# Optimization experiments

Measured on AMD Instinct MI355X. Metric: run time of the kernel, lower is better.

## Reference

```python
import jax, jax.numpy as jnp
import numpy as np
from jax import lax

LAG_SEQ = np.array([1, 2, 3, 7, 14, 28])   # original lags (steps back, newest-first indexing)
MAX_LAG = 28
N_LAGS = LAG_SEQ.size
CTX = 168          # context_length
H_PRED = 24        # prediction horizon H
HID = 512          # LSTM hidden dim
C_IN = 3           # raw channels: target + 2 covariates
IN_DIM = C_IN + 1 + N_LAGS   # + log(scale) feature + lag features = 10
OUT_DIM = 1
B = 512
L = MAX_LAG + CTX + H_PRED - 1   # 219


def setup_inputs() -> dict:
    key = jax.random.key(0)
    ks = jax.random.split(key, 9)
    s = 1.0 / np.sqrt(HID)
    u = lambda k, shape: jax.random.uniform(k, shape, jnp.float32, -s, s)
    return {
        "X": jax.random.normal(ks[0], (B, L, C_IN), jnp.float32),
        "pad_mask": jnp.ones((B, L), jnp.bool_),
        "H": H_PRED,
        "context_length": CTX,
        "W_ih0": u(ks[1], (4 * HID, IN_DIM)),
        "W_hh0": u(ks[2], (4 * HID, HID)),
        "b0": u(ks[3], (4 * HID,)),
        "W_ih1": u(ks[4], (4 * HID, HID)),
        "W_hh1": u(ks[5], (4 * HID, HID)),
        "b1": u(ks[6], (4 * HID,)),
        "W_head": u(ks[7], (HID, OUT_DIM)),
        "b_head": u(ks[8], (OUT_DIM,)),
    }


def _cell(x, h, c, W_ih, W_hh, b):
    # standard torch LSTM cell, gate order i,f,g,o
    g = x @ W_ih.T + h @ W_hh.T + b
    i, f, gg, o = jnp.split(g, 4, axis=-1)
    c = jax.nn.sigmoid(f) * c + jax.nn.sigmoid(i) * jnp.tanh(gg)
    h = jax.nn.sigmoid(o) * jnp.tanh(c)
    return h, c


def reference(X, pad_mask, H, context_length, W_ih0, W_hh0, b0, W_ih1, W_hh1, b1, W_head, b_head):
    Bx = X.shape[0]
    ctx = context_length
    h_steps = H - 1
    # zero out future targets (feature 0); covariates stay known in the future
    X = X.at[:, -h_steps:, 0].set(0.0)
    past = X[:, : X.shape[1] - h_steps, 0][:, ::-1]      # [B, MAX_LAG+ctx], newest-first
    Xs = X[:, MAX_LAG:]                                  # [B, T, C_IN], T = ctx + H - 1
    T = Xs.shape[1]
    m = pad_mask[:, MAX_LAG:][:, :ctx].astype(Xs.dtype)
    # masked mean-abs scaling over the context window of the target channel
    scale = (jnp.abs(Xs[:, :ctx, 0]) * m).sum(1) / jnp.maximum(m.sum(1), 1.0)
    scale = jnp.maximum(scale, 1e-3)[:, None, None]      # [B,1,1]
    past = past / scale[:, :, 0]
    Xcat = jnp.concatenate(
        [Xs[:, :, :1] / scale, Xs[:, :, 1:], jnp.broadcast_to(jnp.log(scale), (Bx, T, 1))],
        axis=2,
    )                                                    # [B, T, C_IN+1]
    # encoder lag features (vectorized create_lags + flip):
    # row i gathers newest-first past at indices LAG_SEQ + (ctx-1-i)
    idx = (ctx - 1 - np.arange(ctx))[:, None] + LAG_SEQ[None, :]   # [ctx, N_LAGS]
    lags = past[:, idx]                                  # [B, ctx, N_LAGS]
    enc_in = jnp.concatenate([Xcat[:, :ctx], lags], axis=2)        # [B, ctx, IN_DIM]

    z = jnp.zeros((Bx, HID), X.dtype)

    def enc_step(carry, x_t):
        h1, c1, h2, c2 = carry
        h1, c1 = _cell(x_t, h1, c1, W_ih0, W_hh0, b0)
        h2, c2 = _cell(h1, h2, c2, W_ih1, W_hh1, b1)
        return (h1, c1, h2, c2), h2

    carry, hs = lax.scan(enc_step, (z, z, z, z), enc_in.transpose(1, 0, 2))
    y_enc = hs.transpose(1, 0, 2) @ W_head + b_head      # [B, ctx, 1]

    covs = Xcat[:, ctx:, 1:].transpose(1, 0, 2)          # [H-1, B, C_IN]
    buf0 = past[:, : MAX_LAG + 1]                        # newest-first target buffer

    def dec_step(carry, cov_t):
        h1, c1, h2, c2, buf, pred = carry
        buf = jnp.concatenate([pred[:, None], buf[:, :-1]], axis=1)
        lag = buf[:, LAG_SEQ]                            # [B, N_LAGS]
        x_t = jnp.concatenate([pred[:, None], cov_t, lag], axis=1)  # [B, IN_DIM]
        h1, c1 = _cell(x_t, h1, c1, W_ih0, W_hh0, b0)
        h2, c2 = _cell(h1, h2, c2, W_ih1, W_hh1, b1)
        y = h2 @ W_head + b_head                         # [B, 1]
        return (h1, c1, h2, c2, buf, y[:, 0]), y

    _, ys = lax.scan(dec_step, (*carry, buf0, y_enc[:, -1, 0]), covs)
    y_dec = ys.transpose(1, 0, 2)                        # [B, H-1, 1]
    return jnp.concatenate([y_enc, y_dec], axis=1) * scale
```

## Files before the change

### kernel.cpp

```cpp
#include <hip/hip_runtime.h>

typedef unsigned short u16;
typedef unsigned int   u32;
typedef __bf16 bf16x8 __attribute__((ext_vector_type(8)));
typedef float  f32x4  __attribute__((ext_vector_type(4)));
static_assert(sizeof(bf16x8) == 16, "bf16x8 size");

#define NL   219
#define NOUT 191

__device__ const int LAGS[6] = {1, 2, 3, 7, 14, 28};

#define OFF_P0H 0UL
#define OFF_P0L (OFF_P0H + 2097152UL)
#define OFF_P1H (OFF_P0L + 2097152UL)
#define OFF_P1L (OFF_P1H + 4194304UL)
#define OFF_H1H (OFF_P1L + 4194304UL)
#define OFF_H1L (OFF_H1H + 1048576UL)
#define OFF_H2H (OFF_H1L + 1048576UL)
#define OFF_H2L (OFF_H2H + 1048576UL)
#define OFF_H2F (OFF_H2L + 1048576UL)
#define OFF_C1  (OFF_H2F + 2097152UL)
#define OFF_C2  (OFF_C1  + 1048576UL)
#define OFF_XF  (OFF_C2  + 1048576UL)
#define OFF_SC  (OFF_XF  + 3440640UL)
#define OFF_LS  (OFF_SC  + 2048UL)
#define OFF_VAL (OFF_LS  + 2048UL)
#define WS_NEED (OFF_VAL + 106496UL)
#define HPAR 262144UL

#define WSPTRS \
  u16*  p0h = (u16*)(ws + OFF_P0H); \
  u16*  p0l = (u16*)(ws + OFF_P0L); \
  u16*  p1h = (u16*)(ws + OFF_P1H); \
  u16*  p1l = (u16*)(ws + OFF_P1L); \
  u16*  h1h = (u16*)(ws + OFF_H1H); \
  u16*  h1l = (u16*)(ws + OFF_H1L); \
  u16*  h2h = (u16*)(ws + OFF_H2H); \
  u16*  h2l = (u16*)(ws + OFF_H2L); \
  float* h2f = (float*)(ws + OFF_H2F); \
  float* c1  = (float*)(ws + OFF_C1); \
  float* c2  = (float*)(ws + OFF_C2); \
  float* xf  = (float*)(ws + OFF_XF); \
  float* scp = (float*)(ws + OFF_SC); \
  float* lsp = (float*)(ws + OFF_LS); \
  float* valp = (float*)(ws + OFF_VAL); \
  (void)p0h;(void)p0l;(void)p1h;(void)p1l;(void)h1h;(void)h1l;(void)h2h;(void)h2l; \
  (void)h2f;(void)c1;(void)c2;(void)xf;(void)scp;(void)lsp;(void)valp;

__device__ __forceinline__ float sigm(float x){ return 1.f / (1.f + __expf(-x)); }
__device__ __forceinline__ float tanhx(float x){
  float ax = fabsf(x);
  float t  = __expf(-2.f * ax);
  float r  = (1.f - t) / (1.f + t);
  return copysignf(r, x);
}
__device__ __forceinline__ u16 f2bf(float x){
  u32 u = __float_as_uint(x);
  return (u16)((u + 0x7FFFu + ((u >> 16) & 1u)) >> 16);
}
__device__ __forceinline__ float bf2f(u16 h){ return __uint_as_float(((u32)h) << 16); }

template<int MF, int KB>
__device__ __forceinline__ void cell_mfma(
    const u16* __restrict__ AhiA, const u16* __restrict__ AloA,
    const u16* __restrict__ AhiB, const u16* __restrict__ AloB,
    const u16* __restrict__ phi,  const u16* __restrict__ plo,
    int R0, int jt, const float* __restrict__ bias,
    f32x4 (&acc)[MF][4])
{
  const int lane = threadIdx.x & 63;
  const int lrow = lane & 15;
  #pragma unroll
  for (int nf = 0; nf < 4; nf++){
    float bv = bias[nf * 512 + jt * 16 + lrow];
    f32x4 v = {bv, bv, bv, bv};
    #pragma unroll
    for (int mf = 0; mf < MF; mf++) acc[mf][nf] = v;
  }
  const size_t alo = (size_t)(lane >> 4) * 8;
  const size_t pb0 = (size_t)(jt * 4) * KB * 512 + (size_t)lane * 8;
  #pragma unroll 2
  for (int kb = 0; kb < KB; kb++){
    const u16* Ah; const u16* Al; int kl;
    if (KB == 16 || kb < 16){ Ah = AhiA; Al = AloA; kl = kb; }
    else                     { Ah = AhiB; Al = AloB; kl = kb - 16; }
    bf16x8 ah[MF], al[MF];
    #pragma unroll
    for (int mf = 0; mf < MF; mf++){
      size_t ao = (size_t)(R0 + mf * 16 + lrow) * 512 + (size_t)kl * 32 + alo;
      ah[mf] = *(const bf16x8*)(Ah + ao);
      al[mf] = *(const bf16x8*)(Al + ao);
    }
    bf16x8 bh[4], bl[4];
    #pragma unroll
    for (int nf = 0; nf < 4; nf++){
      size_t bo = pb0 + ((size_t)nf * KB + kb) * 512;
      bh[nf] = *(const bf16x8*)(phi + bo);
      bl[nf] = *(const bf16x8*)(plo + bo);
    }
    #pragma unroll
    for (int mf = 0; mf < MF; mf++){
      #pragma unroll
      for (int nf = 0; nf < 4; nf++){
        acc[mf][nf] = __builtin_amdgcn_mfma_f32_16x16x32_bf16(ah[mf], bh[nf], acc[mf][nf], 0, 0, 0);
        acc[mf][nf] = __builtin_amdgcn_mfma_f32_16x16x32_bf16(ah[mf], bl[nf], acc[mf][nf], 0, 0, 0);
        acc[mf][nf] = __builtin_amdgcn_mfma_f32_16x16x32_bf16(al[mf], bh[nf], acc[mf][nf], 0, 0, 0);
      }
    }
  }
}

template<int MF, bool XP>
__device__ __forceinline__ void cell_epi(
    f32x4 (&acc)[MF][4], int wrowbase, int m0, int jt,
    const float* xSl, const float* WihSl,
    float* __restrict__ cst,
    u16* __restrict__ hhd, u16* __restrict__ hld, float* __restrict__ hfd)
{
  const int lane = threadIdx.x & 63;
  const int lrow = lane & 15, lkb = lane >> 4;
  const int j = jt * 16 + lrow;
  #pragma unroll
  for (int mf = 0; mf < MF; mf++){
    #pragma unroll
    for (int r = 0; r < 4; r++){
      int lr = wrowbase + mf * 16 + lkb * 4 + r;
      int b  = m0 + lr;
      float gi = acc[mf][0][r], gf = acc[mf][1][r], gg = acc[mf][2][r], go = acc[mf][3][r];
      if (XP){
        #pragma unroll
        for (int k = 0; k < 10; k++){
          float xv = xSl[lr * 10 + k];
          gi += xv * WihSl[(0 * 16 + lrow) * 10 + k];
          gf += xv * WihSl[(1 * 16 + lrow) * 10 + k];
          gg += xv * WihSl[(2 * 16 + lrow) * 10 + k];
          go += xv * WihSl[(3 * 16 + lrow) * 10 + k];
        }
      }
      size_t ci = ((size_t)b << 9) + j;
      float co = cst[ci];
      float cn = sigm(gf) * co + sigm(gi) * tanhx(gg);
      float h  = sigm(go) * tanhx(cn);
      cst[ci] = cn;
      u16 hh = f2bf(h);
      hhd[ci] = hh;
      hld[ci] = f2bf(h - bf2f(hh));
      if (hfd) hfd[ci] = h;
    }
  }
}

__global__ __launch_bounds__(256) void prep1(
    const float* __restrict__ X, const float* __restrict__ Whh0,
    const float* __restrict__ Wih1, const float* __restrict__ Whh1,
    unsigned char* ws)
{
  WSPTRS
  __shared__ float redS[4];
  const int tid = threadIdx.x, w = blockIdx.x;
  const int gtid = w * 256 + tid, G = 65536;
  for (int i = gtid; i < 524288; i += G){ h1h[i] = 0; h1l[i] = 0; h2h[i] = 0; h2l[i] = 0; h2f[i] = 0.f; }
  for (int i = gtid; i < 262144; i += G){ c1[i] = 0.f; c2[i] = 0.f; }
  {
    int rowb = w * 2 + (tid >> 7);
    int t0 = tid & 127;
    float a = fabsf(X[((size_t)rowb * NL + 28 + t0) * 3]);
    if (t0 < 40) a += fabsf(X[((size_t)rowb * NL + 156 + t0) * 3]);
    #pragma unroll
    for (int off = 1; off < 64; off <<= 1) a += __shfl_xor(a, off, 64);
    if ((tid & 63) == 0) redS[tid >> 6] = a;
    __syncthreads();
    if (tid == 0 || tid == 128){
      float s = redS[tid >> 6] + redS[(tid >> 6) + 1];
      float sc = fmaxf(s / 168.f, 0.001f);
      scp[rowb] = sc; lsp[rowb] = logf(sc);
    }
  }
  for (int idx = gtid; idx < 1048576; idx += G){
    int e = idx & 7, ln = (idx >> 3) & 63, kb = (idx >> 9) & 15, nt = idx >> 13;
    int n = (nt & 3) * 512 + (nt >> 2) * 16 + (ln & 15);
    int k = kb * 32 + (ln >> 4) * 8 + e;
    float wv = Whh0[(size_t)n * 512 + k];
    u16 hh = f2bf(wv);
    p0h[idx] = hh; p0l[idx] = f2bf(wv - bf2f(hh));
  }
  for (int idx = gtid; idx < 2097152; idx += G){
    int e = idx & 7, ln = (idx >> 3) & 63, kb = (idx >> 9) & 31, nt = idx >> 14;
    int n = (nt & 3) * 512 + (nt >> 2) * 16 + (ln & 15);
    int k = kb * 32 + (ln >> 4) * 8 + e;
    float wv = (k < 512) ? Wih1[(size_t)n * 512 + k] : Whh1[(size_t)n * 512 + (k - 512)];
    u16 hh = f2bf(wv);
    p1h[idx] = hh; p1l[idx] = f2bf(wv - bf2f(hh));
  }
}

__global__ __launch_bounds__(256) void prep2(const float* __restrict__ X, unsigned char* ws)
{
  WSPTRS
  const int gtid = blockIdx.x * 256 + threadIdx.x, G = 65536;
  for (int idx = gtid; idx < 860160; idx += G){
    int k = idx % 10; int r = idx / 10; int b = r & 511; int t = r >> 9;
    size_t xb = (size_t)b * NL;
    float v;
    if (k == 0)      v = X[(xb + 28 + t) * 3] / scp[b];
    else if (k < 3)  v = X[(xb + 28 + t) * 3 + k];
    else if (k == 3) v = lsp[b];
    else { int lag = LAGS[k - 4]; v = X[(xb + 28 + t - lag) * 3] / scp[b]; }
    xf[idx] = v;
  }
  for (int idx = gtid; idx < 512 * 28; idx += G){
    int b = idx / 28, v = idx % 28;
    valp[b * 52 + v] = X[((size_t)b * NL + 168 + v) * 3] / scp[b];
  }
}

__global__ __launch_bounds__(256) void enc_step(
    const float* __restrict__ Wih0, const float* __restrict__ b0,
    const float* __restrict__ b1,   const float* __restrict__ Whead,
    const float* __restrict__ bhead, float* __restrict__ out,
    unsigned char* ws, int p)
{
  WSPTRS
  __shared__ float xS[1280];
  __shared__ float WihS[640];
  __shared__ float WhS[512];
  const int tid = threadIdx.x, w = blockIdx.x, wave = tid >> 6, jt = w & 31;
  const int P = p & 1;
  if (w < 128){
    const int m0 = ((w >> 5) & 3) * 128;
    if ((w & 31) == 0 && p >= 2){
      for (int i = tid; i < 512; i += 256) WhS[i] = Whead[i];
      __syncthreads();
      int t = p - 2;
      int row = tid >> 1, q = tid & 1;
      int b = m0 + row;
      const float4* h4 = (const float4*)(h2f + (size_t)P * HPAR + ((size_t)b << 9) + q * 256);
      const float4* w4 = (const float4*)(WhS + q * 256);
      float s = 0.f;
      #pragma unroll 8
      for (int i = 0; i < 64; i++){ float4 a = h4[i], bw = w4[i]; s += a.x*bw.x + a.y*bw.y + a.z*bw.z + a.w*bw.w; }
      s += __shfl_xor(s, 1, 64);
      if (q == 0) out[(size_t)b * NOUT + t] = (s + bhead[0]) * scp[b];
    }
    if (p <= 167){
      for (int i = tid; i < 640; i += 256){
        int col = i / 10, k = i % 10;
        int n = (col >> 4) * 512 + jt * 16 + (col & 15);
        WihS[i] = Wih0[n * 10 + k];
      }
      for (int i = tid; i < 1280; i += 256) xS[i] = xf[(size_t)(p * 512 + m0) * 10 + i];
      __syncthreads();
      f32x4 acc[2][4];
      cell_mfma<2,16>(h1h + (size_t)(1 - P) * HPAR, h1l + (size_t)(1 - P) * HPAR, nullptr, nullptr,
                      p0h, p0l, m0 + wave * 32, jt, b0, acc);
      cell_epi<2,true>(acc, wave * 32, m0, jt, xS, WihS, c1,
                       h1h + (size_t)P * HPAR, h1l + (size_t)P * HPAR, nullptr);
    }
  } else {
    if (p >= 1){
      const int m0 = ((w >> 5) & 3) * 128;
      f32x4 acc[2][4];
      cell_mfma<2,32>(h1h + (size_t)(1 - P) * HPAR, h1l + (size_t)(1 - P) * HPAR,
                      h2h + (size_t)P * HPAR,       h2l + (size_t)P * HPAR,
                      p1h, p1l, m0 + wave * 32, jt, b1, acc);
      cell_epi<2,false>(acc, wave * 32, m0, jt, nullptr, nullptr, c2,
                        h2h + (size_t)(1 - P) * HPAR, h2l + (size_t)(1 - P) * HPAR,
                        h2f + (size_t)(1 - P) * HPAR);
    }
  }
}

__global__ __launch_bounds__(256) void dec_cell0(
    const float* __restrict__ X, const float* __restrict__ Wih0,
    const float* __restrict__ b0, const float* __restrict__ Whead,
    const float* __restrict__ bhead, float* __restrict__ out,
    unsigned char* ws, int d)
{
  WSPTRS
  __shared__ float xS[640];
  __shared__ float WihS[640];
  __shared__ float WhS[512];
  __shared__ float ylds[64];
  const int tid = threadIdx.x, w = blockIdx.x, wave = tid >> 6, jt = w & 31;
  const int m0 = (w >> 5) * 64;
  const int hp = (d + 1) & 1;
  for (int i = tid; i < 512; i += 256) WhS[i] = Whead[i];
  for (int i = tid; i < 640; i += 256){
    int col = i / 10, k = i % 10;
    int n = (col >> 4) * 512 + jt * 16 + (col & 15);
    WihS[i] = Wih0[n * 10 + k];
  }
  __syncthreads();
  {
    int row = tid >> 2, q = tid & 3;
    int b = m0 + row;
    const float4* h4 = (const float4*)(h2f + (size_t)hp * HPAR + ((size_t)b << 9) + q * 128);
    const float4* w4 = (const float4*)(WhS + q * 128);
    float s = 0.f;
    #pragma unroll 8
    for (int i = 0; i < 32; i++){ float4 a = h4[i], bw = w4[i]; s += a.x*bw.x + a.y*bw.y + a.z*bw.z + a.w*bw.w; }
    s += __shfl_xor(s, 1, 64); s += __shfl_xor(s, 2, 64);
    if (q == 0){
      float y = s + bhead[0];
      ylds[row] = y;
      if (jt == 0){
        out[(size_t)b * NOUT + 167 + d] = y * scp[b];
        valp[b * 52 + 28 + d] = y;
      }
    }
  }
  __syncthreads();
  if (tid < 64){
    int b = m0 + tid;
    size_t xb = (size_t)b * NL;
    float* xr = xS + tid * 10;
    xr[0] = ylds[tid];
    xr[1] = X[(xb + 196 + d) * 3 + 1];
    xr[2] = X[(xb + 196 + d) * 3 + 2];
    xr[3] = lsp[b];
    #pragma unroll
    for (int j2 = 0; j2 < 6; j2++) xr[4 + j2] = valp[b * 52 + 28 + d - LAGS[j2]];
  }
  __syncthreads();
  f32x4 acc[1][4];
  cell_mfma<1,16>(h1h + (size_t)hp * HPAR, h1l + (size_t)hp * HPAR, nullptr, nullptr,
                  p0h, p0l, m0 + wave * 16, jt, b0, acc);
  cell_epi<1,true>(acc, wave * 16, m0, jt, xS, WihS, c1,
                   h1h + (size_t)(d & 1) * HPAR, h1l + (size_t)(d & 1) * HPAR, nullptr);
}

__global__ __launch_bounds__(256) void dec_cell1(
    const float* __restrict__ b1, unsigned char* ws, int d)
{
  WSPTRS
  const int tid = threadIdx.x, w = blockIdx.x, wave = tid >> 6, jt = w & 31;
  const int m0 = (w >> 5) * 64;
  const int hp = (d + 1) & 1;
  f32x4 acc[1][4];
  cell_mfma<1,32>(h1h + (size_t)(d & 1) * HPAR, h1l + (size_t)(d & 1) * HPAR,
                  h2h + (size_t)hp * HPAR,      h2l + (size_t)hp * HPAR,
                  p1h, p1l, m0 + wave * 16, jt, b1, acc);
  cell_epi<1,false>(acc, wave * 16, m0, jt, nullptr, nullptr, c2,
                    h2h + (size_t)(d & 1) * HPAR, h2l + (size_t)(d & 1) * HPAR,
                    h2f + (size_t)(d & 1) * HPAR);
  (void)tid;
}

__global__ __launch_bounds__(256) void dec_headf(
    const float* __restrict__ Whead, const float* __restrict__ bhead,
    float* __restrict__ out, unsigned char* ws)
{
  WSPTRS
  __shared__ float WhS[512];
  const int tid = threadIdx.x;
  const int m0 = blockIdx.x * 64;
  for (int i = tid; i < 512; i += 256) WhS[i] = Whead[i];
  __syncthreads();
  int row = tid >> 2, q = tid & 3;
  int b = m0 + row;
  const float4* h4 = (const float4*)(h2f + ((size_t)b << 9) + q * 128);
  const float4* w4 = (const float4*)(WhS + q * 128);
  float s = 0.f;
  #pragma unroll 8
  for (int i = 0; i < 32; i++){ float4 a = h4[i], bw = w4[i]; s += a.x*bw.x + a.y*bw.y + a.z*bw.z + a.w*bw.w; }
  s += __shfl_xor(s, 1, 64); s += __shfl_xor(s, 2, 64);
  if (q == 0) out[(size_t)b * NOUT + 190] = (s + bhead[0]) * scp[b];
}

extern "C" void kernel_launch(void* const* d_in, const int* in_sizes, int n_in,
                              void* d_out, int out_size, void* d_ws, size_t ws_size,
                              hipStream_t stream) {
  (void)in_sizes; (void)n_in; (void)out_size;
  if (ws_size < WS_NEED) return;
  const float* X    = (const float*)d_in[0];
  const float* Wih0 = (const float*)d_in[4];
  const float* Whh0 = (const float*)d_in[5];
  const float* b0   = (const float*)d_in[6];
  const float* Wih1 = (const float*)d_in[7];
  const float* Whh1 = (const float*)d_in[8];
  const float* b1   = (const float*)d_in[9];
  const float* Wh   = (const float*)d_in[10];
  const float* bh   = (const float*)d_in[11];
  float* out = (float*)d_out;
  unsigned char* ws = (unsigned char*)d_ws;

  prep1<<<dim3(256), dim3(256), 0, stream>>>(X, Whh0, Wih1, Whh1, ws);
  prep2<<<dim3(256), dim3(256), 0, stream>>>(X, ws);
  for (int p = 0; p <= 168; p++)
    enc_step<<<dim3(256), dim3(256), 0, stream>>>(Wih0, b0, b1, Wh, bh, out, ws, p);
  for (int d = 0; d <= 22; d++){
    dec_cell0<<<dim3(256), dim3(256), 0, stream>>>(X, Wih0, b0, Wh, bh, out, ws, d);
    dec_cell1<<<dim3(256), dim3(256), 0, stream>>>(b1, ws, d);
  }
  dec_headf<<<dim3(8), dim3(256), 0, stream>>>(Wh, bh, out, ws);
}
```

Before: 7.255 ms.

## Fuse all LSTM steps into one persistent kernel with grid barriers and LDS-resident weights

Replaces about 215 per-timestep kernel launches with a single persistent 256-block kernel that advances the encoder and decoder steps using a software grid barrier built on atomics. Each block keeps its slice of the recurrent weights in LDS (all of layer 0, the hi half of layer 1) and holds the cell state in registers instead of global memory. The decoder now uses 2 M-fragments per wave, the same as the encoder. The aim is to remove launch overhead and repeated weight and cell-state traffic. In exchange it depends on all 256 blocks being co-resident, and the barrier has a spin timeout that could break correctness if it expires.

```diff
diff --git a/kernel.cpp b/kernel.cpp
--- a/kernel.cpp
+++ b/kernel.cpp
@@ -20,33 +20,13 @@
 #define OFF_H2H (OFF_H1L + 1048576UL)
 #define OFF_H2L (OFF_H2H + 1048576UL)
 #define OFF_H2F (OFF_H2L + 1048576UL)
-#define OFF_C1  (OFF_H2F + 2097152UL)
-#define OFF_C2  (OFF_C1  + 1048576UL)
-#define OFF_XF  (OFF_C2  + 1048576UL)
+#define OFF_XF  (OFF_H2F + 2097152UL)
 #define OFF_SC  (OFF_XF  + 3440640UL)
 #define OFF_LS  (OFF_SC  + 2048UL)
 #define OFF_VAL (OFF_LS  + 2048UL)
-#define WS_NEED (OFF_VAL + 106496UL)
+#define OFF_BAR (OFF_VAL + 106496UL)
+#define WS_NEED (OFF_BAR + 64UL)
 #define HPAR 262144UL
-
-#define WSPTRS \
-  u16*  p0h = (u16*)(ws + OFF_P0H); \
-  u16*  p0l = (u16*)(ws + OFF_P0L); \
-  u16*  p1h = (u16*)(ws + OFF_P1H); \
-  u16*  p1l = (u16*)(ws + OFF_P1L); \
-  u16*  h1h = (u16*)(ws + OFF_H1H); \
-  u16*  h1l = (u16*)(ws + OFF_H1L); \
-  u16*  h2h = (u16*)(ws + OFF_H2H); \
-  u16*  h2l = (u16*)(ws + OFF_H2L); \
-  float* h2f = (float*)(ws + OFF_H2F); \
-  float* c1  = (float*)(ws + OFF_C1); \
-  float* c2  = (float*)(ws + OFF_C2); \
-  float* xf  = (float*)(ws + OFF_XF); \
-  float* scp = (float*)(ws + OFF_SC); \
-  float* lsp = (float*)(ws + OFF_LS); \
-  float* valp = (float*)(ws + OFF_VAL); \
-  (void)p0h;(void)p0l;(void)p1h;(void)p1l;(void)h1h;(void)h1l;(void)h2h;(void)h2l; \
-  (void)h2f;(void)c1;(void)c2;(void)xf;(void)scp;(void)lsp;(void)valp;
 
 __device__ __forceinline__ float sigm(float x){ return 1.f / (1.f + __expf(-x)); }
 __device__ __forceinline__ float tanhx(float x){
@@ -61,33 +41,53 @@
 }
 __device__ __forceinline__ float bf2f(u16 h){ return __uint_as_float(((u32)h) << 16); }
 
-template<int MF, int KB>
-__device__ __forceinline__ void cell_mfma(
+__device__ __forceinline__ void gridbar(u32* bar, u32 target){
+  __syncthreads();
+  if (threadIdx.x == 0){
+    __threadfence();
+    u32 a = __hip_atomic_fetch_add(bar, 1u, __ATOMIC_ACQ_REL, __HIP_MEMORY_SCOPE_AGENT);
+    if (a == 255u){
+      __hip_atomic_store(bar, 0u, __ATOMIC_RELAXED, __HIP_MEMORY_SCOPE_AGENT);
+      __hip_atomic_fetch_add(bar + 1, 1u, __ATOMIC_RELEASE, __HIP_MEMORY_SCOPE_AGENT);
+    } else {
+      u32 sp = 0;
+      while (__hip_atomic_load(bar + 1, __ATOMIC_ACQUIRE, __HIP_MEMORY_SCOPE_AGENT) < target
+             && ++sp < (1u << 17))
+        __builtin_amdgcn_s_sleep(2);
+    }
+    __threadfence();
+  }
+  __syncthreads();
+}
+
+template<int KB>
+__device__ __forceinline__ void cell_mfma2(
     const u16* __restrict__ AhiA, const u16* __restrict__ AloA,
     const u16* __restrict__ AhiB, const u16* __restrict__ AloB,
-    const u16* __restrict__ phi,  const u16* __restrict__ plo,
-    int R0, int jt, const float* __restrict__ bias,
-    f32x4 (&acc)[MF][4])
+    const u16* bh_s, const u16* bl_s,
+    int R0, float4 bias4, f32x4 (&acc)[2][4])
 {
   const int lane = threadIdx.x & 63;
   const int lrow = lane & 15;
-  #pragma unroll
-  for (int nf = 0; nf < 4; nf++){
-    float bv = bias[nf * 512 + jt * 16 + lrow];
-    f32x4 v = {bv, bv, bv, bv};
-    #pragma unroll
-    for (int mf = 0; mf < MF; mf++) acc[mf][nf] = v;
+  {
+    const float* bp = (const float*)&bias4;
+    #pragma unroll
+    for (int nf = 0; nf < 4; nf++){
+      float bv = bp[nf];
+      f32x4 v = {bv, bv, bv, bv};
+      acc[0][nf] = v; acc[1][nf] = v;
+    }
   }
   const size_t alo = (size_t)(lane >> 4) * 8;
-  const size_t pb0 = (size_t)(jt * 4) * KB * 512 + (size_t)lane * 8;
-  #pragma unroll 2
+  const u32 bo0 = (u32)lane * 8;
+  #pragma unroll 4
   for (int kb = 0; kb < KB; kb++){
     const u16* Ah; const u16* Al; int kl;
     if (KB == 16 || kb < 16){ Ah = AhiA; Al = AloA; kl = kb; }
     else                     { Ah = AhiB; Al = AloB; kl = kb - 16; }
-    bf16x8 ah[MF], al[MF];
-    #pragma unroll
-    for (int mf = 0; mf < MF; mf++){
+    bf16x8 ah[2], al[2];
+    #pragma unroll
+    for (int mf = 0; mf < 2; mf++){
       size_t ao = (size_t)(R0 + mf * 16 + lrow) * 512 + (size_t)kl * 32 + alo;
       ah[mf] = *(const bf16x8*)(Ah + ao);
       al[mf] = *(const bf16x8*)(Al + ao);
@@ -95,12 +95,12 @@
     bf16x8 bh[4], bl[4];
     #pragma unroll
     for (int nf = 0; nf < 4; nf++){
-      size_t bo = pb0 + ((size_t)nf * KB + kb) * 512;
-      bh[nf] = *(const bf16x8*)(phi + bo);
-      bl[nf] = *(const bf16x8*)(plo + bo);
-    }
-    #pragma unroll
-    for (int mf = 0; mf < MF; mf++){
+      u32 off = ((u32)(nf * KB + kb) << 9) + bo0;
+      bh[nf] = *(const bf16x8*)(bh_s + off);
+      bl[nf] = *(const bf16x8*)(bl_s + off);
+    }
+    #pragma unroll
+    for (int mf = 0; mf < 2; mf++){
       #pragma unroll
       for (int nf = 0; nf < 4; nf++){
         acc[mf][nf] = __builtin_amdgcn_mfma_f32_16x16x32_bf16(ah[mf], bh[nf], acc[mf][nf], 0, 0, 0);
@@ -111,18 +111,17 @@
   }
 }
 
-template<int MF, bool XP>
-__device__ __forceinline__ void cell_epi(
-    f32x4 (&acc)[MF][4], int wrowbase, int m0, int jt,
+template<bool XP>
+__device__ __forceinline__ void cell_epi2(
+    f32x4 (&acc)[2][4], float (&creg)[8], int wrowbase, int m0, int jt,
     const float* xSl, const float* WihSl,
-    float* __restrict__ cst,
     u16* __restrict__ hhd, u16* __restrict__ hld, float* __restrict__ hfd)
 {
   const int lane = threadIdx.x & 63;
   const int lrow = lane & 15, lkb = lane >> 4;
   const int j = jt * 16 + lrow;
   #pragma unroll
-  for (int mf = 0; mf < MF; mf++){
+  for (int mf = 0; mf < 2; mf++){
     #pragma unroll
     for (int r = 0; r < 4; r++){
       int lr = wrowbase + mf * 16 + lkb * 4 + r;
@@ -138,11 +137,11 @@
           go += xv * WihSl[(3 * 16 + lrow) * 10 + k];
         }
       }
-      size_t ci = ((size_t)b << 9) + j;
-      float co = cst[ci];
+      float co = creg[mf * 4 + r];
       float cn = sigm(gf) * co + sigm(gi) * tanhx(gg);
       float h  = sigm(go) * tanhx(cn);
-      cst[ci] = cn;
+      creg[mf * 4 + r] = cn;
+      size_t ci = ((size_t)b << 9) + j;
       u16 hh = f2bf(h);
       hhd[ci] = hh;
       hld[ci] = f2bf(h - bf2f(hh));
@@ -151,17 +150,63 @@
   }
 }
 
-__global__ __launch_bounds__(256) void prep1(
-    const float* __restrict__ X, const float* __restrict__ Whh0,
+__global__ void initbar(unsigned char* ws){
+  if (threadIdx.x < 16) ((u32*)(ws + OFF_BAR))[threadIdx.x] = 0;
+}
+
+__global__ __launch_bounds__(256, 1) void deepar(
+    const float* __restrict__ X,    const float* __restrict__ Wih0,
+    const float* __restrict__ Whh0, const float* __restrict__ b0,
     const float* __restrict__ Wih1, const float* __restrict__ Whh1,
+    const float* __restrict__ b1,   const float* __restrict__ Whead,
+    const float* __restrict__ bhead, float* __restrict__ out,
     unsigned char* ws)
 {
-  WSPTRS
+  __shared__ u16   BW[65536];
+  __shared__ float xS[1280];
+  __shared__ float WihS[640];
+  __shared__ float WhS[512];
+  __shared__ float ylds[128];
   __shared__ float redS[4];
-  const int tid = threadIdx.x, w = blockIdx.x;
-  const int gtid = w * 256 + tid, G = 65536;
+
+  u16*  p0h = (u16*)(ws + OFF_P0H);
+  u16*  p0l = (u16*)(ws + OFF_P0L);
+  u16*  p1h = (u16*)(ws + OFF_P1H);
+  u16*  p1l = (u16*)(ws + OFF_P1L);
+  u16*  h1h = (u16*)(ws + OFF_H1H);
+  u16*  h1l = (u16*)(ws + OFF_H1L);
+  u16*  h2h = (u16*)(ws + OFF_H2H);
+  u16*  h2l = (u16*)(ws + OFF_H2L);
+  float* h2f = (float*)(ws + OFF_H2F);
+  float* xf  = (float*)(ws + OFF_XF);
+  float* scp = (float*)(ws + OFF_SC);
+  float* lsp = (float*)(ws + OFF_LS);
+  float* valp = (float*)(ws + OFF_VAL);
+  u32*  bar = (u32*)(ws + OFF_BAR);
+
+  const int tid  = threadIdx.x;
+  const int w    = blockIdx.x;
+  const int wave = tid >> 6;
+  const int jt   = w & 31;
+  const int m0   = ((w >> 5) & 3) * 128;
+  const int G    = 65536;
+  const int gtid = w * 256 + tid;
+  u32 bcnt = 0;
+
+  float creg[8];
+  #pragma unroll
+  for (int i = 0; i < 8; i++) creg[i] = 0.f;
+
+  float4 bias4;
+  {
+    const float* bb = (w < 128) ? b0 : b1;
+    int c = jt * 16 + (tid & 15);
+    bias4.x = bb[0 * 512 + c]; bias4.y = bb[1 * 512 + c];
+    bias4.z = bb[2 * 512 + c]; bias4.w = bb[3 * 512 + c];
+  }
+  const float bheadv = bhead[0];
+
   for (int i = gtid; i < 524288; i += G){ h1h[i] = 0; h1l[i] = 0; h2h[i] = 0; h2l[i] = 0; h2f[i] = 0.f; }
-  for (int i = gtid; i < 262144; i += G){ c1[i] = 0.f; c2[i] = 0.f; }
   {
     int rowb = w * 2 + (tid >> 7);
     int t0 = tid & 127;
@@ -193,12 +238,8 @@
     u16 hh = f2bf(wv);
     p1h[idx] = hh; p1l[idx] = f2bf(wv - bf2f(hh));
   }
-}
-
-__global__ __launch_bounds__(256) void prep2(const float* __restrict__ X, unsigned char* ws)
-{
-  WSPTRS
-  const int gtid = blockIdx.x * 256 + threadIdx.x, G = 65536;
+  gridbar(bar, ++bcnt);
+
   for (int idx = gtid; idx < 860160; idx += G){
     int k = idx % 10; int r = idx / 10; int b = r & 511; int t = r >> 9;
     size_t xb = (size_t)b * NL;
@@ -213,159 +254,126 @@
     int b = idx / 28, v = idx % 28;
     valp[b * 52 + v] = X[((size_t)b * NL + 168 + v) * 3] / scp[b];
   }
-}
-
-__global__ __launch_bounds__(256) void enc_step(
-    const float* __restrict__ Wih0, const float* __restrict__ b0,
-    const float* __restrict__ b1,   const float* __restrict__ Whead,
-    const float* __restrict__ bhead, float* __restrict__ out,
-    unsigned char* ws, int p)
-{
-  WSPTRS
-  __shared__ float xS[1280];
-  __shared__ float WihS[640];
-  __shared__ float WhS[512];
-  const int tid = threadIdx.x, w = blockIdx.x, wave = tid >> 6, jt = w & 31;
-  const int P = p & 1;
   if (w < 128){
-    const int m0 = ((w >> 5) & 3) * 128;
-    if ((w & 31) == 0 && p >= 2){
-      for (int i = tid; i < 512; i += 256) WhS[i] = Whead[i];
+    const uint4* sh = (const uint4*)(p0h + (size_t)jt * 32768);
+    const uint4* sl = (const uint4*)(p0l + (size_t)jt * 32768);
+    uint4* dB = (uint4*)BW;
+    for (int i = tid; i < 4096; i += 256){ dB[i] = sh[i]; dB[4096 + i] = sl[i]; }
+    for (int i = tid; i < 640; i += 256){
+      int col = i / 10, k = i % 10;
+      int n = (col >> 4) * 512 + jt * 16 + (col & 15);
+      WihS[i] = Wih0[n * 10 + k];
+    }
+    for (int i = tid; i < 512; i += 256) WhS[i] = Whead[i];
+  } else {
+    const uint4* sh = (const uint4*)(p1h + (size_t)jt * 65536);
+    uint4* dB = (uint4*)BW;
+    for (int i = tid; i < 8192; i += 256) dB[i] = sh[i];
+  }
+  gridbar(bar, ++bcnt);
+
+  for (int p = 0; p <= 168; p++){
+    const int P = p & 1;
+    if (w < 128){
+      if ((w & 31) == 0 && p >= 2){
+        int t = p - 2;
+        int row = tid >> 1, q = tid & 1;
+        int b = m0 + row;
+        const float4* h4 = (const float4*)(h2f + (size_t)P * HPAR + ((size_t)b << 9) + q * 256);
+        const float4* w4 = (const float4*)(WhS + q * 256);
+        float s = 0.f;
+        #pragma unroll 8
+        for (int i = 0; i < 64; i++){ float4 a = h4[i], bw = w4[i]; s += a.x*bw.x + a.y*bw.y + a.z*bw.z + a.w*bw.w; }
+        s += __shfl_xor(s, 1, 64);
+        if (q == 0) out[(size_t)b * NOUT + t] = (s + bheadv) * scp[b];
+      }
+      if (p <= 167){
+        for (int i = tid; i < 1280; i += 256) xS[i] = xf[(size_t)(p * 512 + m0) * 10 + i];
+        __syncthreads();
+        f32x4 acc[2][4];
+        cell_mfma2<16>(h1h + (size_t)(1 - P) * HPAR, h1l + (size_t)(1 - P) * HPAR, nullptr, nullptr,
+                       BW, BW + 32768, m0 + wave * 32, bias4, acc);
+        cell_epi2<true>(acc, creg, wave * 32, m0, jt, xS, WihS,
+                        h1h + (size_t)P * HPAR, h1l + (size_t)P * HPAR, nullptr);
+      }
+    } else {
+      if (p >= 1){
+        f32x4 acc[2][4];
+        cell_mfma2<32>(h1h + (size_t)(1 - P) * HPAR, h1l + (size_t)(1 - P) * HPAR,
+                       h2h + (size_t)P * HPAR,       h2l + (size_t)P * HPAR,
+                       BW, p1l + (size_t)jt * 65536, m0 + wave * 32, bias4, acc);
+        cell_epi2<false>(acc, creg, wave * 32, m0, jt, nullptr, nullptr,
+                         h2h + (size_t)(1 - P) * HPAR, h2l + (size_t)(1 - P) * HPAR,
+                         h2f + (size_t)(1 - P) * HPAR);
+      }
+    }
+    gridbar(bar, ++bcnt);
+  }
+
+  for (int d = 0; d <= 22; d++){
+    const int hp = (d + 1) & 1;
+    if (w < 128){
+      {
+        int row = tid >> 1, q = tid & 1;
+        int b = m0 + row;
+        const float4* h4 = (const float4*)(h2f + (size_t)hp * HPAR + ((size_t)b << 9) + q * 256);
+        const float4* w4 = (const float4*)(WhS + q * 256);
+        float s = 0.f;
+        #pragma unroll 8
+        for (int i = 0; i < 64; i++){ float4 a = h4[i], bw = w4[i]; s += a.x*bw.x + a.y*bw.y + a.z*bw.z + a.w*bw.w; }
+        s += __shfl_xor(s, 1, 64);
+        if (q == 0){
+          float y = s + bheadv;
+          ylds[row] = y;
+          if (jt == 0){
+            out[(size_t)b * NOUT + 167 + d] = y * scp[b];
+            valp[b * 52 + 28 + d] = y;
+          }
+        }
+      }
       __syncthreads();
-      int t = p - 2;
-      int row = tid >> 1, q = tid & 1;
-      int b = m0 + row;
-      const float4* h4 = (const float4*)(h2f + (size_t)P * HPAR + ((size_t)b << 9) + q * 256);
-      const float4* w4 = (const float4*)(WhS + q * 256);
-      float s = 0.f;
-      #pragma unroll 8
-      for (int i = 0; i < 64; i++){ float4 a = h4[i], bw = w4[i]; s += a.x*bw.x + a.y*bw.y + a.z*bw.z + a.w*bw.w; }
-      s += __shfl_xor(s, 1, 64);
-      if (q == 0) out[(size_t)b * NOUT + t] = (s + bhead[0]) * scp[b];
-    }
-    if (p <= 167){
-      for (int i = tid; i < 640; i += 256){
-        int col = i / 10, k = i % 10;
-        int n = (col >> 4) * 512 + jt * 16 + (col & 15);
-        WihS[i] = Wih0[n * 10 + k];
-      }
-      for (int i = tid; i < 1280; i += 256) xS[i] = xf[(size_t)(p * 512 + m0) * 10 + i];
+      if (tid < 128){
+        int b = m0 + tid;
+        size_t xb = (size_t)b * NL;
+        float* xr = xS + tid * 10;
+        xr[0] = ylds[tid];
+        xr[1] = X[(xb + 196 + d) * 3 + 1];
+        xr[2] = X[(xb + 196 + d) * 3 + 2];
+        xr[3] = lsp[b];
+        #pragma unroll
+        for (int j2 = 0; j2 < 6; j2++) xr[4 + j2] = valp[b * 52 + 28 + d - LAGS[j2]];
+      }
       __syncthreads();
       f32x4 acc[2][4];
-      cell_mfma<2,16>(h1h + (size_t)(1 - P) * HPAR, h1l + (size_t)(1 - P) * HPAR, nullptr, nullptr,
-                      p0h, p0l, m0 + wave * 32, jt, b0, acc);
-      cell_epi<2,true>(acc, wave * 32, m0, jt, xS, WihS, c1,
-                       h1h + (size_t)P * HPAR, h1l + (size_t)P * HPAR, nullptr);
-    }
-  } else {
-    if (p >= 1){
-      const int m0 = ((w >> 5) & 3) * 128;
+      cell_mfma2<16>(h1h + (size_t)hp * HPAR, h1l + (size_t)hp * HPAR, nullptr, nullptr,
+                     BW, BW + 32768, m0 + wave * 32, bias4, acc);
+      cell_epi2<true>(acc, creg, wave * 32, m0, jt, xS, WihS,
+                      h1h + (size_t)(d & 1) * HPAR, h1l + (size_t)(d & 1) * HPAR, nullptr);
+    }
+    gridbar(bar, ++bcnt);
+    if (w >= 128){
       f32x4 acc[2][4];
-      cell_mfma<2,32>(h1h + (size_t)(1 - P) * HPAR, h1l + (size_t)(1 - P) * HPAR,
-                      h2h + (size_t)P * HPAR,       h2l + (size_t)P * HPAR,
-                      p1h, p1l, m0 + wave * 32, jt, b1, acc);
-      cell_epi<2,false>(acc, wave * 32, m0, jt, nullptr, nullptr, c2,
-                        h2h + (size_t)(1 - P) * HPAR, h2l + (size_t)(1 - P) * HPAR,
-                        h2f + (size_t)(1 - P) * HPAR);
-    }
-  }
-}
-
-__global__ __launch_bounds__(256) void dec_cell0(
-    const float* __restrict__ X, const float* __restrict__ Wih0,
-    const float* __restrict__ b0, const float* __restrict__ Whead,
-    const float* __restrict__ bhead, float* __restrict__ out,
-    unsigned char* ws, int d)
-{
-  WSPTRS
-  __shared__ float xS[640];
-  __shared__ float WihS[640];
-  __shared__ float WhS[512];
-  __shared__ float ylds[64];
-  const int tid = threadIdx.x, w = blockIdx.x, wave = tid >> 6, jt = w & 31;
-  const int m0 = (w >> 5) * 64;
-  const int hp = (d + 1) & 1;
-  for (int i = tid; i < 512; i += 256) WhS[i] = Whead[i];
-  for (int i = tid; i < 640; i += 256){
-    int col = i / 10, k = i % 10;
-    int n = (col >> 4) * 512 + jt * 16 + (col & 15);
-    WihS[i] = Wih0[n * 10 + k];
-  }
-  __syncthreads();
-  {
-    int row = tid >> 2, q = tid & 3;
+      cell_mfma2<32>(h1h + (size_t)(d & 1) * HPAR, h1l + (size_t)(d & 1) * HPAR,
+                     h2h + (size_t)hp * HPAR,      h2l + (size_t)hp * HPAR,
+                     BW, p1l + (size_t)jt * 65536, m0 + wave * 32, bias4, acc);
+      cell_epi2<false>(acc, creg, wave * 32, m0, jt, nullptr, nullptr,
+                       h2h + (size_t)(d & 1) * HPAR, h2l + (size_t)(d & 1) * HPAR,
+                       h2f + (size_t)(d & 1) * HPAR);
+    }
+    gridbar(bar, ++bcnt);
+  }
+
+  if (w < 128){
+    int row = tid >> 1, q = tid & 1;
     int b = m0 + row;
-    const float4* h4 = (const float4*)(h2f + (size_t)hp * HPAR + ((size_t)b << 9) + q * 128);
-    const float4* w4 = (const float4*)(WhS + q * 128);
+    const float4* h4 = (const float4*)(h2f + ((size_t)b << 9) + q * 256);
+    const float4* w4 = (const float4*)(WhS + q * 256);
     float s = 0.f;
     #pragma unroll 8
-    for (int i = 0; i < 32; i++){ float4 a = h4[i], bw = w4[i]; s += a.x*bw.x + a.y*bw.y + a.z*bw.z + a.w*bw.w; }
-    s += __shfl_xor(s, 1, 64); s += __shfl_xor(s, 2, 64);
-    if (q == 0){
-      float y = s + bhead[0];
-      ylds[row] = y;
-      if (jt == 0){
-        out[(size_t)b * NOUT + 167 + d] = y * scp[b];
-        valp[b * 52 + 28 + d] = y;
-      }
-    }
-  }
-  __syncthreads();
-  if (tid < 64){
-    int b = m0 + tid;
-    size_t xb = (size_t)b * NL;
-    float* xr = xS + tid * 10;
-    xr[0] = ylds[tid];
-    xr[1] = X[(xb + 196 + d) * 3 + 1];
-    xr[2] = X[(xb + 196 + d) * 3 + 2];
-    xr[3] = lsp[b];
-    #pragma unroll
-    for (int j2 = 0; j2 < 6; j2++) xr[4 + j2] = valp[b * 52 + 28 + d - LAGS[j2]];
-  }
-  __syncthreads();
-  f32x4 acc[1][4];
-  cell_mfma<1,16>(h1h + (size_t)hp * HPAR, h1l + (size_t)hp * HPAR, nullptr, nullptr,
-                  p0h, p0l, m0 + wave * 16, jt, b0, acc);
-  cell_epi<1,true>(acc, wave * 16, m0, jt, xS, WihS, c1,
-                   h1h + (size_t)(d & 1) * HPAR, h1l + (size_t)(d & 1) * HPAR, nullptr);
-}
-
-__global__ __launch_bounds__(256) void dec_cell1(
-    const float* __restrict__ b1, unsigned char* ws, int d)
-{
-  WSPTRS
-  const int tid = threadIdx.x, w = blockIdx.x, wave = tid >> 6, jt = w & 31;
-  const int m0 = (w >> 5) * 64;
-  const int hp = (d + 1) & 1;
-  f32x4 acc[1][4];
-  cell_mfma<1,32>(h1h + (size_t)(d & 1) * HPAR, h1l + (size_t)(d & 1) * HPAR,
-                  h2h + (size_t)hp * HPAR,      h2l + (size_t)hp * HPAR,
-                  p1h, p1l, m0 + wave * 16, jt, b1, acc);
-  cell_epi<1,false>(acc, wave * 16, m0, jt, nullptr, nullptr, c2,
-                    h2h + (size_t)(d & 1) * HPAR, h2l + (size_t)(d & 1) * HPAR,
-                    h2f + (size_t)(d & 1) * HPAR);
-  (void)tid;
-}
-
-__global__ __launch_bounds__(256) void dec_headf(
-    const float* __restrict__ Whead, const float* __restrict__ bhead,
-    float* __restrict__ out, unsigned char* ws)
-{
-  WSPTRS
-  __shared__ float WhS[512];
-  const int tid = threadIdx.x;
-  const int m0 = blockIdx.x * 64;
-  for (int i = tid; i < 512; i += 256) WhS[i] = Whead[i];
-  __syncthreads();
-  int row = tid >> 2, q = tid & 3;
-  int b = m0 + row;
-  const float4* h4 = (const float4*)(h2f + ((size_t)b << 9) + q * 128);
-  const float4* w4 = (const float4*)(WhS + q * 128);
-  float s = 0.f;
-  #pragma unroll 8
-  for (int i = 0; i < 32; i++){ float4 a = h4[i], bw = w4[i]; s += a.x*bw.x + a.y*bw.y + a.z*bw.z + a.w*bw.w; }
-  s += __shfl_xor(s, 1, 64); s += __shfl_xor(s, 2, 64);
-  if (q == 0) out[(size_t)b * NOUT + 190] = (s + bhead[0]) * scp[b];
+    for (int i = 0; i < 64; i++){ float4 a = h4[i], bw = w4[i]; s += a.x*bw.x + a.y*bw.y + a.z*bw.z + a.w*bw.w; }
+    s += __shfl_xor(s, 1, 64);
+    if (q == 0 && jt == 0) out[(size_t)b * NOUT + 190] = (s + bheadv) * scp[b];
+  }
 }
 
 extern "C" void kernel_launch(void* const* d_in, const int* in_sizes, int n_in,
@@ -385,13 +393,6 @@
   float* out = (float*)d_out;
   unsigned char* ws = (unsigned char*)d_ws;
 
-  prep1<<<dim3(256), dim3(256), 0, stream>>>(X, Whh0, Wih1, Whh1, ws);
-  prep2<<<dim3(256), dim3(256), 0, stream>>>(X, ws);
-  for (int p = 0; p <= 168; p++)
-    enc_step<<<dim3(256), dim3(256), 0, stream>>>(Wih0, b0, b1, Wh, bh, out, ws, p);
-  for (int d = 0; d <= 22; d++){
-    dec_cell0<<<dim3(256), dim3(256), 0, stream>>>(X, Wih0, b0, Wh, bh, out, ws, d);
-    dec_cell1<<<dim3(256), dim3(256), 0, stream>>>(b1, ws, d);
-  }
-  dec_headf<<<dim3(8), dim3(256), 0, stream>>>(Wh, bh, out, ws);
-}
+  initbar<<<dim3(1), dim3(64), 0, stream>>>(ws);
+  deepar<<<dim3(256), dim3(256), 0, stream>>>(X, Wih0, Whh0, b0, Wih1, Whh1, b1, Wh, bh, out, ws);
+}
```

Result: slower. 20.61 ms (+184.0%).
